# Kernel tuning notes

Measured on AMD Instinct MI355X. Metric: run time of the kernel, lower is better.

The kernel has to match this reference:

```python
import jax, jax.numpy as jnp
import numpy as np

D_MODEL = 384
N_HEADS = 8
HEAD_DIM = D_MODEL // N_HEADS


def setup_inputs() -> dict:
    key = jax.random.key(0)
    ks = jax.random.split(key, 8)
    b, n = 2, 2048
    s = 0.02
    return {
        "x": jax.random.normal(ks[0], (b, n, D_MODEL), jnp.float32),
        "coords": jax.random.normal(ks[1], (b, n, 3), jnp.float32),
        "W_qkv": jax.random.normal(ks[2], (D_MODEL, 3 * D_MODEL), jnp.float32) * s,
        "b_qkv": jnp.zeros((3 * D_MODEL,), jnp.float32),
        "W_dist": jax.random.normal(ks[3], (1, N_HEADS), jnp.float32) * s,
        "b_dist": jnp.zeros((N_HEADS,), jnp.float32),
        "W_out": jax.random.normal(ks[4], (D_MODEL, D_MODEL), jnp.float32) * s,
        "b_out": jnp.zeros((D_MODEL,), jnp.float32),
    }


def reference(x, coords, W_qkv, b_qkv, W_dist, b_dist, W_out, b_out):
    b, n, _ = x.shape
    qkv = x @ W_qkv + b_qkv                       # (b, n, 3*d)
    q, k, v = jnp.split(qkv, 3, axis=-1)
    def heads(t):
        return t.reshape(b, n, N_HEADS, HEAD_DIM).transpose(0, 2, 1, 3)  # b h n d
    q, k, v = heads(q), heads(k), heads(v)
    attn = jnp.einsum('bhid,bhjd->bhij', q, k) / jnp.sqrt(jnp.float32(HEAD_DIM))
    # distance bias: ||c_i - c_j|| projected to heads (Linear(1, n_heads))
    diff = coords[:, :, None, :] - coords[:, None, :, :]   # (b, i, j, 3)
    dist = jnp.sqrt(jnp.sum(diff * diff, axis=-1))         # (b, i, j)
    dist_bias = dist[..., None] * W_dist[0] + b_dist       # (b, i, j, h)
    attn = attn + dist_bias.transpose(0, 3, 1, 2)          # (b, h, i, j)
    attn = jax.nn.softmax(attn, axis=-1)
    out = jnp.einsum('bhij,bhjd->bhid', attn, v)
    out = out.transpose(0, 2, 1, 3).reshape(b, n, D_MODEL)
    return out @ W_out + b_out
```

## Files before the change

### kernel.cpp

```cpp
#include <hip/hip_runtime.h>
#include <hip/hip_bf16.h>

#define NB 2
#define SEQ 2048
#define DM 384
#define NH 8
#define HD 48
#define QKVN 1152
#define BH (NB*NH)
#define NSPLIT 4

typedef __hip_bfloat16 bf16;
typedef __attribute__((ext_vector_type(8))) short short8;
typedef __attribute__((ext_vector_type(4))) float float4v;

static __device__ __forceinline__ float bf2f(bf16 v){ return __bfloat162float(v); }
static __device__ __forceinline__ float ldin(const void* p, size_t i, int isf){
    return isf ? ((const float*)p)[i] : bf2f(((const bf16*)p)[i]);
}
static __device__ __forceinline__ short f2b(float f){
    union { float f; unsigned u; } a; a.f = f;
    unsigned r = a.u + 0x7FFFu + ((a.u >> 16) & 1u);
    return (short)(r >> 16);
}
static __device__ __forceinline__ unsigned pk2(float a, float b){
    union { float f; unsigned u; } ua, ub; ua.f = a; ub.f = b;
    return ((ua.u + 0x8000u) >> 16) | ((ub.u + 0x8000u) & 0xFFFF0000u);
}
static __device__ __forceinline__ float bflo(unsigned u){
    union { unsigned u; float f; } a; a.u = u << 16; return a.f;
}
static __device__ __forceinline__ float bfhi(unsigned u){
    union { unsigned u; float f; } a; a.u = u & 0xFFFF0000u; return a.f;
}
static __device__ __forceinline__ short8 s4z(int2 v){
    union { int2 i; short s[4]; } u; u.i = v;
    short8 r = {u.s[0], u.s[1], u.s[2], u.s[3], 0, 0, 0, 0};
    return r;
}
static __device__ __forceinline__ short8 u2z(unsigned a, unsigned b){
    union { unsigned u[2]; short s[4]; } u0; u0.u[0] = a; u0.u[1] = b;
    short8 r = {u0.s[0], u0.s[1], u0.s[2], u0.s[3], 0, 0, 0, 0};
    return r;
}
static __device__ __forceinline__ int detect_isf(const void* x){
    const unsigned short* xb = (const unsigned short*)x;
    int l = threadIdx.x & 63;
    union { unsigned u; float f; } a; a.u = ((unsigned)xb[2*l]) << 16;
    float ab = fabsf(a.f);
    int good = (a.f == 0.0f) || (ab > 9.765625e-4f && ab < 1024.0f);
    unsigned long long m = __ballot(good);
    return (__popcll(m) >= 32) ? 0 : 1;
}

__global__ __launch_bounds__(256) void k_prep(const void* __restrict__ x,
    const void* __restrict__ coords,
    const void* __restrict__ Wqkv, const void* __restrict__ Wout,
    const void* __restrict__ bqkv, const void* __restrict__ bout,
    const void* __restrict__ Wdist, const void* __restrict__ bdist,
    short* __restrict__ dist8, short* __restrict__ xb,
    short* __restrict__ WqT, short* __restrict__ WoT,
    float* __restrict__ bqf, float* __restrict__ bof,
    float* __restrict__ wdf, float* __restrict__ bdf)
{
    const int isf = detect_isf(x);
    const int t = threadIdx.x;
    const int b = blockIdx.x;
    if (b < 256) {
        const int bb = b >> 7;
        const int j0 = (b & 127) * 16;
        __shared__ float cjx[16], cjy[16], cjz[16];
        if (t < 16) {
            int gj = (bb*SEQ + j0 + t)*3;
            cjx[t] = ldin(coords, gj, isf);
            cjy[t] = ldin(coords, gj+1, isf);
            cjz[t] = ldin(coords, gj+2, isf);
        }
        __syncthreads();
        #pragma unroll
        for (int k = 0; k < 8; ++k) {
            int i = k*256 + t;
            int gi = (bb*SEQ + i)*3;
            float px = ldin(coords, gi, isf), py = ldin(coords, gi+1, isf), pz = ldin(coords, gi+2, isf);
            short o[16];
            #pragma unroll
            for (int e = 0; e < 16; ++e) {
                float dx = px - cjx[e], dy = py - cjy[e], dz = pz - cjz[e];
                o[e] = f2b(sqrtf(dx*dx + dy*dy + dz*dz));
            }
            short* dst = dist8 + ((size_t)b*SEQ + i)*16;
            *(int4*)dst       = *(const int4*)(o);
            *(int4*)(dst + 8) = *(const int4*)(o + 8);
        }
    } else if (b < 1024) {
        size_t i = ((size_t)(b-256)*256 + t)*8;
        if (isf) {
            const float* xf = (const float*)x + i;
            short o[8];
            #pragma unroll
            for (int e = 0; e < 8; ++e) o[e] = f2b(xf[e]);
            *(int4*)(xb + i) = *(const int4*)o;
        } else {
            *(int4*)(xb + i) = *(const int4*)((const short*)x + i);
        }
    } else if (b < 1600) {
        int bb, NW; const void* W; short* WT;
        if (b < 1456) { bb = b - 1024; NW = QKVN; W = Wqkv; WT = WqT; }
        else          { bb = b - 1456; NW = DM;   W = Wout; WT = WoT; }
        int ntiles = NW >> 5;
        int kt = bb / ntiles, nt = bb % ntiles;
        int k0 = kt*32, n0 = nt*32;
        __shared__ float Ls[32][33];
        for (int idx = t; idx < 1024; idx += 256) {
            int r = idx >> 5, c = idx & 31;
            Ls[r][c] = ldin(W, (size_t)(k0+r)*NW + n0 + c, isf);
        }
        __syncthreads();
        for (int idx = t; idx < 1024; idx += 256) {
            int r2 = idx >> 5, c2 = idx & 31;
            WT[(size_t)(n0+r2)*DM + k0 + c2] = f2b(Ls[c2][r2]);
        }
    } else {
        int idx = (b - 1600)*256 + t;
        const float log2e = 1.4426950408889634f;
        if (idx < QKVN) bqf[idx] = ldin(bqkv, idx, isf);
        else if (idx < QKVN + DM) bof[idx - QKVN] = ldin(bout, idx - QKVN, isf);
        else if (idx < QKVN + DM + NH) wdf[idx - QKVN - DM] = ldin(Wdist, idx - QKVN - DM, isf)*log2e;
        else if (idx < QKVN + DM + 2*NH) bdf[idx - QKVN - DM - NH] = ldin(bdist, idx - QKVN - DM - NH, isf)*log2e;
    }
}

__global__ __launch_bounds__(256) void k_qkv(const short* __restrict__ xb,
    const short* __restrict__ WT, const float* __restrict__ bias,
    short* __restrict__ qg2, short* __restrict__ kg2, short* __restrict__ vg2)
{
    __shared__ __align__(16) short As[64*72];
    __shared__ __align__(16) short Bs[128*72];
    const int t = threadIdx.x;
    const int w = t >> 6, lane = t & 63, L = lane & 15, quad = lane >> 4;
    const int mt = blockIdx.x / 9, nt = blockIdx.x % 9;
    const int row0 = mt*64, col0 = nt*128;
    const int wm = w & 1, wn = w >> 1;
    float4v acc[2][4] = {};
    for (int k0 = 0; k0 < DM; k0 += 64) {
        __syncthreads();
        for (int c = t; c < 512; c += 256) {
            int row = c >> 3, k8 = c & 7;
            *(int4*)(&As[row*72 + k8*8]) = *(const int4*)(xb + (size_t)(row0+row)*DM + k0 + k8*8);
        }
        for (int c = t; c < 1024; c += 256) {
            int row = c >> 3, k8 = c & 7;
            *(int4*)(&Bs[row*72 + k8*8]) = *(const int4*)(WT + (size_t)(col0+row)*DM + k0 + k8*8);
        }
        __syncthreads();
        #pragma unroll
        for (int kc = 0; kc < 2; ++kc) {
            short8 a0 = *(const short8*)(&As[(32*wm + L)*72 + kc*32 + quad*8]);
            short8 a1 = *(const short8*)(&As[(32*wm + 16 + L)*72 + kc*32 + quad*8]);
            #pragma unroll
            for (int ni = 0; ni < 4; ++ni) {
                short8 bf = *(const short8*)(&Bs[(64*wn + 16*ni + L)*72 + kc*32 + quad*8]);
                acc[0][ni] = __builtin_amdgcn_mfma_f32_16x16x32_bf16(a0, bf, acc[0][ni], 0, 0, 0);
                acc[1][ni] = __builtin_amdgcn_mfma_f32_16x16x32_bf16(a1, bf, acc[1][ni], 0, 0, 0);
            }
        }
    }
    const int which = col0 / DM;
    const int cbase = col0 % DM;
    short* Ep = Bs;
    __syncthreads();
    if (which < 2) {
        #pragma unroll
        for (int mi = 0; mi < 2; ++mi)
            #pragma unroll
            for (int ni = 0; ni < 4; ++ni) {
                int col_l = 64*wn + 16*ni + L;
                float bv = bias[col0 + col_l];
                #pragma unroll
                for (int r = 0; r < 4; ++r) {
                    int row_l = 32*wm + 16*mi + quad*4 + r;
                    Ep[row_l*136 + col_l] = f2b(acc[mi][ni][r] + bv);
                }
            }
        __syncthreads();
        short* dst = which ? kg2 : qg2;
        for (int c = t; c < 1024; c += 256) {
            int row_l = c >> 4, col_l = (c & 15)*8;
            int row_g = row0 + row_l;
            int bi = row_g >> 11, nn = row_g & (SEQ-1);
            int c2 = cbase + col_l;
            int hh = c2/HD, dh = c2%HD;
            int bh = bi*NH + hh;
            size_t base = ((size_t)bh*128 + (nn>>4))*768;
            int Ltok = nn & 15;
            const short* src = &Ep[row_l*136 + col_l];
            if (dh < 32) {
                *(int4*)(dst + base + (dh>>3)*128 + Ltok*8) = *(const int4*)src;
            } else {
                int q0 = (dh - 32) >> 2;
                *(int2*)(dst + base + 512 + q0*64     + Ltok*4) = *(const int2*)src;
                *(int2*)(dst + base + 512 + (q0+1)*64 + Ltok*4) = *(const int2*)(src + 4);
            }
        }
    } else {
        #pragma unroll
        for (int mi = 0; mi < 2; ++mi)
            #pragma unroll
            for (int ni = 0; ni < 4; ++ni) {
                int col_l = 64*wn + 16*ni + L;
                float bv = bias[col0 + col_l];
                #pragma unroll
                for (int r = 0; r < 4; ++r) {
                    int row_l = 32*wm + 16*mi + quad*4 + r;
                    Ep[col_l*72 + row_l] = f2b(acc[mi][ni][r] + bv);
                }
            }
        __syncthreads();
        for (int c = t; c < 1024; c += 256) {
            int col_l = c >> 3, row8 = (c & 7)*8;
            int row_g = row0 + row8;
            int bi = row_g >> 11, nn = row_g & (SEQ-1);
            int c2 = cbase + col_l;
            int hh = c2/HD, dh = c2%HD;
            int bh = bi*NH + hh;
            int dt = dh >> 4, Lh = dh & 15;
            size_t base3 = (((size_t)bh*128 + (nn>>4))*3 + dt)*256;
            int q0 = (nn & 15) >> 2;
            const short* src = &Ep[col_l*72 + row8];
            *(int2*)(vg2 + base3 + q0*64     + Lh*4) = *(const int2*)src;
            *(int2*)(vg2 + base3 + (q0+1)*64 + Lh*4) = *(const int2*)(src + 4);
        }
    }
}

__global__ __launch_bounds__(256, 3) void k_attn(
    const short* __restrict__ qg2, const short* __restrict__ kg2, const short* __restrict__ vg2,
    const short* __restrict__ dist8, const float* __restrict__ wdf,
    const float* __restrict__ bdf, short* __restrict__ partO, float* __restrict__ partL)
{
    __shared__ float Ored[2][64*48];
    __shared__ float Lred[2][64];
    const int t = threadIdx.x;
    const int w = t >> 6, lane = t & 63, L = lane & 15, q = lane >> 4;
    const int bid = blockIdx.x;
    const int jsb = bid & 3, it = (bid >> 2) & 31, bh = bid >> 7;
    const int bi = bh >> 3, hh = bh & 7;
    const int i0 = it*64;
    const float scale2 = 0.14433756729740643f * 1.4426950408889634f;
    const float wd = wdf[hh], bd = bdf[hh];

    const short* qB = qg2 + ((size_t)bh*128 + it*4)*768;
    short8 qa0[4], qa1[4];
    #pragma unroll
    for (int nt = 0; nt < 4; ++nt) {
        qa0[nt] = *(const short8*)(qB + nt*768 + q*128 + L*8);
        qa1[nt] = s4z(*(const int2*)(qB + nt*768 + 512 + q*64 + L*4));
    }

    float4v accO[4][3] = {};
    float rsum[4] = {};

    const short* kBp = kg2 + ((size_t)bh*128 + jsb*32 + w)*768;
    const short* vBp = vg2 + ((size_t)bh*128 + jsb*32 + w)*768;
    const short* dBp = dist8 + (((size_t)bi*128 + jsb*32 + w)*SEQ + i0 + L)*16 + 4*q;

    #pragma unroll 2
    for (int itr = 0; itr < SEQ/NSPLIT/64; ++itr) {
        short8 ka0 = *(const short8*)(kBp + q*128 + L*8);
        short8 ka1 = s4z(*(const int2*)(kBp + 512 + q*64 + L*4));
        float4v sacc[4] = {};
        #pragma unroll
        for (int nt = 0; nt < 4; ++nt) {
            sacc[nt] = __builtin_amdgcn_mfma_f32_16x16x32_bf16(ka0, qa0[nt], sacc[nt], 0, 0, 0);
            sacc[nt] = __builtin_amdgcn_mfma_f32_16x16x32_bf16(ka1, qa1[nt], sacc[nt], 0, 0, 0);
        }
        short8 vf[3];
        #pragma unroll
        for (int dt = 0; dt < 3; ++dt)
            vf[dt] = s4z(*(const int2*)(vBp + dt*256 + q*64 + L*4));
        short8 pa[4];
        #pragma unroll
        for (int nt = 0; nt < 4; ++nt) {
            int2 du = *(const int2*)(dBp + nt*256);
            float d0 = bflo((unsigned)du.x), d1 = bfhi((unsigned)du.x);
            float d2 = bflo((unsigned)du.y), d3 = bfhi((unsigned)du.y);
            float p0 = __builtin_amdgcn_exp2f(fmaf(sacc[nt][0], scale2, fmaf(d0, wd, bd)));
            float p1 = __builtin_amdgcn_exp2f(fmaf(sacc[nt][1], scale2, fmaf(d1, wd, bd)));
            float p2 = __builtin_amdgcn_exp2f(fmaf(sacc[nt][2], scale2, fmaf(d2, wd, bd)));
            float p3 = __builtin_amdgcn_exp2f(fmaf(sacc[nt][3], scale2, fmaf(d3, wd, bd)));
            rsum[nt] += (p0 + p1) + (p2 + p3);
            pa[nt] = u2z(pk2(p0, p1), pk2(p2, p3));
        }
        #pragma unroll
        for (int nt = 0; nt < 4; ++nt)
            #pragma unroll
            for (int dt = 0; dt < 3; ++dt)
                accO[nt][dt] = __builtin_amdgcn_mfma_f32_16x16x32_bf16(pa[nt], vf[dt], accO[nt][dt], 0, 0, 0);
        kBp += 4*768; vBp += 4*768; dBp += (size_t)4*SEQ*16;
    }
    #pragma unroll
    for (int nt = 0; nt < 4; ++nt) {
        rsum[nt] += __shfl_xor(rsum[nt], 16);
        rsum[nt] += __shfl_xor(rsum[nt], 32);
    }
    if (w >= 2) {
        float* Od = Ored[w-2];
        #pragma unroll
        for (int mt = 0; mt < 4; ++mt)
            #pragma unroll
            for (int dt = 0; dt < 3; ++dt)
                #pragma unroll
                for (int r = 0; r < 4; ++r)
                    Od[(16*mt + 4*q + r)*48 + 16*dt + L] = accO[mt][dt][r];
        if (q == 0)
            #pragma unroll
            for (int nt = 0; nt < 4; ++nt) Lred[w-2][16*nt + L] = rsum[nt];
    }
    __syncthreads();
    if (w < 2) {
        float* Od = Ored[w];
        #pragma unroll
        for (int mt = 0; mt < 4; ++mt)
            #pragma unroll
            for (int dt = 0; dt < 3; ++dt)
                #pragma unroll
                for (int r = 0; r < 4; ++r)
                    accO[mt][dt][r] += Od[(16*mt + 4*q + r)*48 + 16*dt + L];
        #pragma unroll
        for (int nt = 0; nt < 4; ++nt) rsum[nt] += Lred[w][16*nt + L];
    }
    __syncthreads();
    if (w == 1) {
        float* Od = Ored[0];
        #pragma unroll
        for (int mt = 0; mt < 4; ++mt)
            #pragma unroll
            for (int dt = 0; dt < 3; ++dt)
                #pragma unroll
                for (int r = 0; r < 4; ++r)
                    Od[(16*mt + 4*q + r)*48 + 16*dt + L] = accO[mt][dt][r];
        if (q == 0)
            #pragma unroll
            for (int nt = 0; nt < 4; ++nt) Lred[0][16*nt + L] = rsum[nt];
    }
    __syncthreads();
    if (w == 0) {
        float* Od = Ored[0];
        const size_t pbase = ((size_t)(jsb*BH + bh))*SEQ;
        #pragma unroll
        for (int mt = 0; mt < 4; ++mt)
            #pragma unroll
            for (int dt = 0; dt < 3; ++dt)
                #pragma unroll
                for (int r = 0; r < 4; ++r) {
                    float v = accO[mt][dt][r] + Od[(16*mt + 4*q + r)*48 + 16*dt + L];
                    partO[(pbase + i0 + 16*mt + 4*q + r)*48 + 16*dt + L] = f2b(v);
                }
        if (q == 0)
            #pragma unroll
            for (int nt = 0; nt < 4; ++nt)
                partL[pbase + i0 + 16*nt + L] = rsum[nt] + Lred[0][16*nt + L];
    }
}

__global__ __launch_bounds__(256) void k_red(const short* __restrict__ partO,
    const float* __restrict__ partL, short* __restrict__ aob)
{
    int g = blockIdx.x*256 + threadIdx.x;
    int row = g / 48, cg = g % 48;
    int bi = row >> 11, i = row & (SEQ-1);
    int hh = cg / 6, d8 = (cg % 6)*8;
    int bh = bi*NH + hh;
    float acc[8] = {};
    float l = 0.f;
    #pragma unroll
    for (int s = 0; s < NSPLIT; ++s) {
        const short* p = partO + ((size_t)(s*BH + bh)*SEQ + i)*48 + d8;
        uint4 u = *(const uint4*)p;
        acc[0] += bflo(u.x); acc[1] += bfhi(u.x);
        acc[2] += bflo(u.y); acc[3] += bfhi(u.y);
        acc[4] += bflo(u.z); acc[5] += bfhi(u.z);
        acc[6] += bflo(u.w); acc[7] += bfhi(u.w);
        l += partL[(size_t)(s*BH + bh)*SEQ + i];
    }
    float inv = 1.0f / l;
    short o[8];
    #pragma unroll
    for (int e = 0; e < 8; ++e) o[e] = f2b(acc[e]*inv);
    *(int4*)(aob + (size_t)row*DM + hh*HD + d8) = *(const int4*)o;
}

__global__ __launch_bounds__(256) void k_out(const short* __restrict__ aob,
    const short* __restrict__ WT, const float* __restrict__ bias,
    void* __restrict__ out, const void* __restrict__ x)
{
    __shared__ __align__(16) short As[64*72];
    __shared__ __align__(16) short Bs[128*72];
    const int isf = detect_isf(x);
    const int t = threadIdx.x;
    const int w = t >> 6, lane = t & 63, L = lane & 15, quad = lane >> 4;
    const int mt = blockIdx.x / 3, nt = blockIdx.x % 3;
    const int row0 = mt*64, col0 = nt*128;
    const int wm = w & 1, wn = w >> 1;
    float4v acc[2][4] = {};
    for (int k0 = 0; k0 < DM; k0 += 64) {
        __syncthreads();
        for (int c = t; c < 512; c += 256) {
            int row = c >> 3, k8 = c & 7;
            *(int4*)(&As[row*72 + k8*8]) = *(const int4*)(aob + (size_t)(row0+row)*DM + k0 + k8*8);
        }
        for (int c = t; c < 1024; c += 256) {
            int row = c >> 3, k8 = c & 7;
            *(int4*)(&Bs[row*72 + k8*8]) = *(const int4*)(WT + (size_t)(col0+row)*DM + k0 + k8*8);
        }
        __syncthreads();
        #pragma unroll
        for (int kc = 0; kc < 2; ++kc) {
            short8 a0 = *(const short8*)(&As[(32*wm + L)*72 + kc*32 + quad*8]);
            short8 a1 = *(const short8*)(&As[(32*wm + 16 + L)*72 + kc*32 + quad*8]);
            #pragma unroll
            for (int ni = 0; ni < 4; ++ni) {
                short8 bf = *(const short8*)(&Bs[(64*wn + 16*ni + L)*72 + kc*32 + quad*8]);
                acc[0][ni] = __builtin_amdgcn_mfma_f32_16x16x32_bf16(a0, bf, acc[0][ni], 0, 0, 0);
                acc[1][ni] = __builtin_amdgcn_mfma_f32_16x16x32_bf16(a1, bf, acc[1][ni], 0, 0, 0);
            }
        }
    }
    #pragma unroll
    for (int mi = 0; mi < 2; ++mi) {
        #pragma unroll
        for (int ni = 0; ni < 4; ++ni) {
            int col_g = col0 + 64*wn + 16*ni + L;
            float bv = bias[col_g];
            #pragma unroll
            for (int r = 0; r < 4; ++r) {
                int row_g = row0 + 32*wm + 16*mi + quad*4 + r;
                size_t oi = (size_t)row_g*DM + col_g;
                float val = acc[mi][ni][r] + bv;
                if (isf) ((float*)out)[oi] = val;
                else     ((bf16*)out)[oi]  = __float2bfloat16(val);
            }
        }
    }
}

extern "C" void kernel_launch(void* const* d_in, const int* in_sizes, int n_in,
                              void* d_out, int out_size, void* d_ws, size_t ws_size,
                              hipStream_t stream) {
    const void* x      = d_in[0];
    const void* coords = d_in[1];
    const void* Wqkv   = d_in[2];
    const void* bqkv   = d_in[3];
    const void* Wdist  = d_in[4];
    const void* bdist  = d_in[5];
    const void* Wout   = d_in[6];
    const void* bout   = d_in[7];

    short* qg2   = (short*)d_ws;
    short* kg2   = qg2  + (size_t)1572864;
    short* vg2   = kg2  + (size_t)1572864;
    short* dist8 = vg2  + (size_t)1572864;
    short* aob   = dist8 + (size_t)8388608;
    short* xb    = aob  + (size_t)1572864;
    short* WqT   = xb   + (size_t)1572864;
    short* WoT   = WqT  + (size_t)442368;
    short* partO = WoT  + (size_t)147456;
    float* partL = (float*)(partO + (size_t)6291456);
    float* bqf   = partL + (size_t)131072;
    float* bof   = bqf + QKVN;
    float* wdf   = bof + DM;
    float* bdf   = wdf + NH;

    k_prep<<<dim3(1607), dim3(256), 0, stream>>>(x, coords, Wqkv, Wout, bqkv, bout,
                                                 Wdist, bdist, dist8, xb, WqT, WoT,
                                                 bqf, bof, wdf, bdf);
    k_qkv<<<dim3(64*9), dim3(256), 0, stream>>>(xb, WqT, bqf, qg2, kg2, vg2);
    k_attn<<<dim3(16*32*NSPLIT), dim3(256), 0, stream>>>(qg2, kg2, vg2, dist8, wdf, bdf,
                                                         partO, partL);
    k_red<<<dim3(768), dim3(256), 0, stream>>>(partO, partL, aob);
    k_out<<<dim3(64*3), dim3(256), 0, stream>>>(aob, WoT, bof, d_out, x);
}
```

Before: 165.8 us.

## Fuse split-K attention reduction into output projection GEMM and vectorize partial stores

Removes the separate reduction kernel by having the output projection combine the split partial outputs and normalizers while loading its A tile. The attention epilogue now accumulates both waves' results in shared memory and writes partials with coalesced 16-byte stores. This saves one launch and the round trip through the intermediate buffer. In exchange, each of the three column-tile blocks re-reads the partials, and the A-tile load in the output GEMM now does more work.

```diff
diff --git a/kernel.cpp b/kernel.cpp
--- a/kernel.cpp
+++ b/kernel.cpp
@@ -346,68 +346,77 @@
     __syncthreads();
     if (w == 0) {
         float* Od = Ored[0];
-        const size_t pbase = ((size_t)(jsb*BH + bh))*SEQ;
         #pragma unroll
         for (int mt = 0; mt < 4; ++mt)
             #pragma unroll
             for (int dt = 0; dt < 3; ++dt)
                 #pragma unroll
-                for (int r = 0; r < 4; ++r) {
-                    float v = accO[mt][dt][r] + Od[(16*mt + 4*q + r)*48 + 16*dt + L];
-                    partO[(pbase + i0 + 16*mt + 4*q + r)*48 + 16*dt + L] = f2b(v);
-                }
+                for (int r = 0; r < 4; ++r)
+                    Od[(16*mt + 4*q + r)*48 + 16*dt + L] += accO[mt][dt][r];
         if (q == 0)
             #pragma unroll
-            for (int nt = 0; nt < 4; ++nt)
-                partL[pbase + i0 + 16*nt + L] = rsum[nt] + Lred[0][16*nt + L];
-    }
-}
-
-__global__ __launch_bounds__(256) void k_red(const short* __restrict__ partO,
-    const float* __restrict__ partL, short* __restrict__ aob)
-{
-    int g = blockIdx.x*256 + threadIdx.x;
-    int row = g / 48, cg = g % 48;
-    int bi = row >> 11, i = row & (SEQ-1);
-    int hh = cg / 6, d8 = (cg % 6)*8;
-    int bh = bi*NH + hh;
-    float acc[8] = {};
-    float l = 0.f;
-    #pragma unroll
-    for (int s = 0; s < NSPLIT; ++s) {
-        const short* p = partO + ((size_t)(s*BH + bh)*SEQ + i)*48 + d8;
-        uint4 u = *(const uint4*)p;
-        acc[0] += bflo(u.x); acc[1] += bfhi(u.x);
-        acc[2] += bflo(u.y); acc[3] += bfhi(u.y);
-        acc[4] += bflo(u.z); acc[5] += bfhi(u.z);
-        acc[6] += bflo(u.w); acc[7] += bfhi(u.w);
-        l += partL[(size_t)(s*BH + bh)*SEQ + i];
-    }
-    float inv = 1.0f / l;
-    short o[8];
-    #pragma unroll
-    for (int e = 0; e < 8; ++e) o[e] = f2b(acc[e]*inv);
-    *(int4*)(aob + (size_t)row*DM + hh*HD + d8) = *(const int4*)o;
-}
-
-__global__ __launch_bounds__(256) void k_out(const short* __restrict__ aob,
-    const short* __restrict__ WT, const float* __restrict__ bias,
-    void* __restrict__ out, const void* __restrict__ x)
+            for (int nt = 0; nt < 4; ++nt) Lred[0][16*nt + L] += rsum[nt];
+    }
+    __syncthreads();
+    const size_t pbase = ((size_t)(jsb*BH + bh))*SEQ + i0;
+    for (int c = t; c < 384; c += 256) {
+        int r = c / 6, d8 = (c % 6)*8;
+        const float* src = &Ored[0][r*48 + d8];
+        short o[8];
+        #pragma unroll
+        for (int e = 0; e < 8; ++e) o[e] = f2b(src[e]);
+        *(int4*)(partO + (pbase + r)*48 + d8) = *(const int4*)o;
+    }
+    if (t < 64) partL[pbase + t] = Lred[0][t];
+}
+
+__global__ __launch_bounds__(256) void k_out(const short* __restrict__ partO,
+    const float* __restrict__ partL, const short* __restrict__ WT,
+    const float* __restrict__ bias, void* __restrict__ out, const void* __restrict__ x)
 {
     __shared__ __align__(16) short As[64*72];
     __shared__ __align__(16) short Bs[128*72];
+    __shared__ float Linv[64][8];
     const int isf = detect_isf(x);
     const int t = threadIdx.x;
     const int w = t >> 6, lane = t & 63, L = lane & 15, quad = lane >> 4;
     const int mt = blockIdx.x / 3, nt = blockIdx.x % 3;
     const int row0 = mt*64, col0 = nt*128;
     const int wm = w & 1, wn = w >> 1;
+    for (int idx = t; idx < 512; idx += 256) {
+        int r = idx >> 3, hh = idx & 7;
+        int row_g = row0 + r;
+        int bi = row_g >> 11, i = row_g & (SEQ-1);
+        int bh = bi*NH + hh;
+        float l = 0.f;
+        #pragma unroll
+        for (int s = 0; s < NSPLIT; ++s) l += partL[(size_t)(s*BH + bh)*SEQ + i];
+        Linv[r][hh] = 1.0f / l;
+    }
     float4v acc[2][4] = {};
     for (int k0 = 0; k0 < DM; k0 += 64) {
         __syncthreads();
         for (int c = t; c < 512; c += 256) {
-            int row = c >> 3, k8 = c & 7;
-            *(int4*)(&As[row*72 + k8*8]) = *(const int4*)(aob + (size_t)(row0+row)*DM + k0 + k8*8);
+            int row_l = c >> 3, k8 = c & 7;
+            int kcol = k0 + k8*8;
+            int hh = kcol / HD, d8 = kcol % HD;
+            int row_g = row0 + row_l;
+            int bi = row_g >> 11, i = row_g & (SEQ-1);
+            int bh = bi*NH + hh;
+            float a[8] = {};
+            #pragma unroll
+            for (int s = 0; s < NSPLIT; ++s) {
+                uint4 u = *(const uint4*)(partO + ((size_t)(s*BH + bh)*SEQ + i)*48 + d8);
+                a[0] += bflo(u.x); a[1] += bfhi(u.x);
+                a[2] += bflo(u.y); a[3] += bfhi(u.y);
+                a[4] += bflo(u.z); a[5] += bfhi(u.z);
+                a[6] += bflo(u.w); a[7] += bfhi(u.w);
+            }
+            float inv = Linv[row_l][hh];
+            short o[8];
+            #pragma unroll
+            for (int e = 0; e < 8; ++e) o[e] = f2b(a[e]*inv);
+            *(int4*)(&As[row_l*72 + k8*8]) = *(const int4*)o;
         }
         for (int c = t; c < 1024; c += 256) {
             int row = c >> 3, k8 = c & 7;
@@ -460,8 +469,7 @@
     short* kg2   = qg2  + (size_t)1572864;
     short* vg2   = kg2  + (size_t)1572864;
     short* dist8 = vg2  + (size_t)1572864;
-    short* aob   = dist8 + (size_t)8388608;
-    short* xb    = aob  + (size_t)1572864;
+    short* xb    = dist8 + (size_t)8388608;
     short* WqT   = xb   + (size_t)1572864;
     short* WoT   = WqT  + (size_t)442368;
     short* partO = WoT  + (size_t)147456;
@@ -477,6 +485,5 @@
     k_qkv<<<dim3(64*9), dim3(256), 0, stream>>>(xb, WqT, bqf, qg2, kg2, vg2);
     k_attn<<<dim3(16*32*NSPLIT), dim3(256), 0, stream>>>(qg2, kg2, vg2, dist8, wdf, bdf,
                                                          partO, partL);
-    k_red<<<dim3(768), dim3(256), 0, stream>>>(partO, partL, aob);
-    k_out<<<dim3(64*3), dim3(256), 0, stream>>>(aob, WoT, bof, d_out, x);
-}
+    k_out<<<dim3(64*3), dim3(256), 0, stream>>>(partO, partL, WoT, bof, d_out, x);
+}
```

Result: slower. 172.5 us (+4.0%).
